# Performance work log

Hardware: AMD Instinct MI355X
Metric: run time of the kernel (lower is better)

The kernel has to match this reference:

```python
import jax, jax.numpy as jnp
import numpy as np

N = 100000   # nodes
E = 1000000  # edges
F_IN = 128
H = 64
L = 6
C = 10
G = 64       # graphs in batch


def setup_inputs() -> dict:
    key = jax.random.key(0)
    ks = jax.random.split(key, 12)
    x = jax.random.normal(ks[0], (N, F_IN), dtype=jnp.float32)
    edge_index = jax.random.randint(ks[1], (2, E), 0, N, dtype=jnp.int64)
    batch = jnp.sort(jax.random.randint(ks[2], (N,), 0, G, dtype=jnp.int64))
    s = lambda fan: 1.0 / np.sqrt(fan)
    return {
        "x": x,
        "edge_index": edge_index,
        "batch": batch,
        "W0": jax.random.normal(ks[3], (F_IN, H), dtype=jnp.float32) * s(F_IN),
        "b0": jnp.zeros((H,), jnp.float32),
        "Wh": jax.random.normal(ks[4], (L - 1, H, H), dtype=jnp.float32) * s(H),
        "bh": jnp.zeros((L - 1, H), jnp.float32),
        "jkW": jax.random.normal(ks[5], (H * L, H), dtype=jnp.float32) * s(H * L),
        "jkb": jnp.zeros((H,), jnp.float32),
        "W1": jax.random.normal(ks[6], (H, H), dtype=jnp.float32) * s(H),
        "b1": jnp.zeros((H,), jnp.float32),
        "W2": jax.random.normal(ks[7], (H, C), dtype=jnp.float32) * s(H),
        "b2": jnp.zeros((C,), jnp.float32),
    }


def reference(x, edge_index, batch, W0, b0, Wh, bh, jkW, jkb, W1, b1, W2, b2):
    n = x.shape[0]
    # add self-loops (PyG GCNConv default)
    loops = jnp.arange(n, dtype=edge_index.dtype)
    src = jnp.concatenate([edge_index[0], loops])
    dst = jnp.concatenate([edge_index[1], loops])
    # symmetric degree normalization D^{-1/2} (A+I) D^{-1/2}
    deg = jax.ops.segment_sum(jnp.ones_like(dst, x.dtype), dst, num_segments=n)
    disq = jnp.where(deg > 0, deg ** -0.5, 0.0)
    norm = (disq[src] * disq[dst])[:, None]  # [E+N, 1]

    def gcn(h, W, b):
        hW = h @ W                              # [N, H] transform first
        msg = hW[src] * norm                    # gather + normalize
        agg = jax.ops.segment_sum(msg, dst, num_segments=n)  # scatter-add
        return agg + b

    h = jax.nn.relu(gcn(x, W0, b0))
    xs = [h]
    for i in range(L - 1):
        h = jax.nn.relu(gcn(h, Wh[i], bh[i]))
        xs.append(h)
    hcat = jnp.concatenate(xs, axis=-1)         # JK 'cat' -> [N, H*L]
    h = jax.nn.relu(hcat @ jkW + jkb)
    pooled = jax.ops.segment_sum(h, batch, num_segments=G)  # global_add_pool
    h = jax.nn.relu(pooled @ W1 + b1)
    return jax.nn.softmax(h @ W2 + b2, axis=-1)  # [G, C]
```

## Files before the change

### kernel.cpp

```cpp
#include <hip/hip_runtime.h>
#include <hip/hip_fp16.h>

#define NN 100000
#define NE 1000000
#define F_INF 128
#define HID 64
#define NLAY 6
#define NCLS 10
#define NGRAPH 64
#define PART_SZ 12500
#define SCAT_BLKS (((NE + 2047) / 2048) * 8)
#define GEMM_GRID ((NN + 63) / 64)

typedef float floatx2 __attribute__((ext_vector_type(2)));

__device__ __forceinline__ float4 h4f(ushort4 u) {
    __half2 lo = *reinterpret_cast<__half2*>(&u);
    __half2 hi = *reinterpret_cast<__half2*>(reinterpret_cast<unsigned short*>(&u) + 2);
    float2 a = __half22float2(lo);
    float2 b = __half22float2(hi);
    return make_float4(a.x, a.y, b.x, b.y);
}

__device__ __forceinline__ ushort4 f4h(float4 v) {
    __half2 lo = __floats2half2_rn(v.x, v.y);
    __half2 hi = __floats2half2_rn(v.z, v.w);
    ushort4 u;
    *reinterpret_cast<__half2*>(&u) = lo;
    *reinterpret_cast<__half2*>(reinterpret_cast<unsigned short*>(&u) + 2) = hi;
    return u;
}

__device__ __forceinline__ unsigned f4_fp8(float4 v) {
    unsigned w = 0;
    w = __builtin_amdgcn_cvt_pk_fp8_f32(v.x, v.y, w, false);
    w = __builtin_amdgcn_cvt_pk_fp8_f32(v.z, v.w, w, true);
    return w;
}

__device__ __forceinline__ void accf8(unsigned u, float4& a) {
    floatx2 lo = __builtin_amdgcn_cvt_pk_f32_fp8(u, false);
    floatx2 hi = __builtin_amdgcn_cvt_pk_f32_fp8(u, true);
    a.x += lo[0]; a.y += lo[1]; a.z += hi[0]; a.w += hi[1];
}

__global__ void k_hist(const int* __restrict__ dst, int* __restrict__ counts, int e) {
    int i0 = blockIdx.x * 1024 + threadIdx.x;
    #pragma unroll
    for (int k = 0; k < 4; k++) {
        int i = i0 + k * 256;
        if (i < e) atomicAdd(&counts[dst[i]], 1);
    }
}

__global__ void k_blocksum(const int* __restrict__ counts, int* __restrict__ bsum, int n) {
    int i = blockIdx.x * 256 + threadIdx.x;
    int v = (i < n) ? counts[i] : 0;
    #pragma unroll
    for (int off = 32; off >= 1; off >>= 1) v += __shfl_down(v, off);
    __shared__ int ws[4];
    if ((threadIdx.x & 63) == 0) ws[threadIdx.x >> 6] = v;
    __syncthreads();
    if (threadIdx.x == 0) bsum[blockIdx.x] = ws[0] + ws[1] + ws[2] + ws[3];
}

__global__ void k_scanbsum(int* __restrict__ bsum, int nb) {
    __shared__ int sh[512];
    int t = threadIdx.x;
    int v = (t < nb) ? bsum[t] : 0;
    sh[t] = v; __syncthreads();
    for (int off = 1; off < 512; off <<= 1) {
        int x = (t >= off) ? sh[t - off] : 0;
        __syncthreads();
        sh[t] += x; __syncthreads();
    }
    if (t < nb) bsum[t] = sh[t] - v;
}

__global__ void k_scanwrite(const int* __restrict__ counts, const int* __restrict__ bsumx,
                            int* __restrict__ rowptr, int* __restrict__ wptr,
                            float* __restrict__ disq, int n, int e) {
    __shared__ int sh[256];
    int t = threadIdx.x;
    int i = blockIdx.x * 256 + t;
    int v = (i < n) ? counts[i] : 0;
    sh[t] = v; __syncthreads();
    for (int off = 1; off < 256; off <<= 1) {
        int x = (t >= off) ? sh[t - off] : 0;
        __syncthreads();
        sh[t] += x; __syncthreads();
    }
    int excl = sh[t] - v + bsumx[blockIdx.x];
    if (i < n) {
        rowptr[i] = excl;
        wptr[i]   = excl;
        disq[i]   = rsqrtf((float)(v + 1));
    }
    if (i == 0) rowptr[n] = e;
}

__global__ __launch_bounds__(256) void k_scatter_gemm0(
    const int* __restrict__ src, const int* __restrict__ dst,
    int* __restrict__ wptr, int* __restrict__ csr, int e,
    const float* __restrict__ x, const float* __restrict__ W0,
    const float* __restrict__ disq, unsigned* __restrict__ C8, int n)
{
    __shared__ float Ws[32 * 64];
    __shared__ float As[64 * 36];

    if (blockIdx.x >= GEMM_GRID) {
        int sbid = blockIdx.x - GEMM_GRID;
        int part = sbid & 7;
        int i0 = (sbid >> 3) * 2048 + threadIdx.x;
        #pragma unroll
        for (int k = 0; k < 8; k++) {
            int i = i0 + k * 256;
            if (i < e) {
                int d = dst[i];
                if (d / PART_SZ == part) {
                    int pos = atomicAdd(&wptr[d], 1);
                    csr[pos] = src[i];
                }
            }
        }
        return;
    }

    const int tid  = threadIdx.x;
    const int col4 = (tid & 15) * 4;
    const int rowq = tid >> 4;
    const int base = blockIdx.x * 64;
    const int ar   = tid >> 3;
    const int ac4  = (tid & 7) * 4;

    float4 wreg[2], areg[2];
    #pragma unroll
    for (int i = 0; i < 2; i++)
        wreg[i] = *(const float4*)(W0 + (size_t)(i * 256 + tid) * 4);
    #pragma unroll
    for (int rr = 0; rr < 2; rr++) {
        int row = base + ar + rr * 32;
        areg[rr] = make_float4(0.f, 0.f, 0.f, 0.f);
        if (row < n) areg[rr] = *(const float4*)(x + (size_t)row * F_INF + ac4);
    }
    #pragma unroll
    for (int i = 0; i < 2; i++)
        *(float4*)(Ws + (size_t)(i * 256 + tid) * 4) = wreg[i];
    #pragma unroll
    for (int rr = 0; rr < 2; rr++)
        *(float4*)(As + (size_t)(ar + rr * 32) * 36 + ac4) = areg[rr];
    __syncthreads();

    float4 acc[4];
    #pragma unroll
    for (int r = 0; r < 4; r++) acc[r] = make_float4(0.f, 0.f, 0.f, 0.f);

    for (int k0 = 0; k0 < F_INF; k0 += 32) {
        const bool more = (k0 + 32) < F_INF;
        if (more) {
            #pragma unroll
            for (int i = 0; i < 2; i++)
                wreg[i] = *(const float4*)(W0 + (size_t)(k0 + 32) * 64 + (i * 256 + tid) * 4);
            #pragma unroll
            for (int rr = 0; rr < 2; rr++) {
                int row = base + ar + rr * 32;
                areg[rr] = make_float4(0.f, 0.f, 0.f, 0.f);
                if (row < n) areg[rr] = *(const float4*)(x + (size_t)row * F_INF + k0 + 32 + ac4);
            }
        }
        #pragma unroll 8
        for (int k = 0; k < 32; k++) {
            float4 w = *(const float4*)(Ws + k * 64 + col4);
            float a0 = As[(rowq * 4 + 0) * 36 + k];
            float a1 = As[(rowq * 4 + 1) * 36 + k];
            float a2 = As[(rowq * 4 + 2) * 36 + k];
            float a3 = As[(rowq * 4 + 3) * 36 + k];
            acc[0].x = fmaf(a0, w.x, acc[0].x); acc[0].y = fmaf(a0, w.y, acc[0].y);
            acc[0].z = fmaf(a0, w.z, acc[0].z); acc[0].w = fmaf(a0, w.w, acc[0].w);
            acc[1].x = fmaf(a1, w.x, acc[1].x); acc[1].y = fmaf(a1, w.y, acc[1].y);
            acc[1].z = fmaf(a1, w.z, acc[1].z); acc[1].w = fmaf(a1, w.w, acc[1].w);
            acc[2].x = fmaf(a2, w.x, acc[2].x); acc[2].y = fmaf(a2, w.y, acc[2].y);
            acc[2].z = fmaf(a2, w.z, acc[2].z); acc[2].w = fmaf(a2, w.w, acc[2].w);
            acc[3].x = fmaf(a3, w.x, acc[3].x); acc[3].y = fmaf(a3, w.y, acc[3].y);
            acc[3].z = fmaf(a3, w.z, acc[3].z); acc[3].w = fmaf(a3, w.w, acc[3].w);
        }
        __syncthreads();
        if (more) {
            #pragma unroll
            for (int i = 0; i < 2; i++)
                *(float4*)(Ws + (size_t)(i * 256 + tid) * 4) = wreg[i];
            #pragma unroll
            for (int rr = 0; rr < 2; rr++)
                *(float4*)(As + (size_t)(ar + rr * 32) * 36 + ac4) = areg[rr];
            __syncthreads();
        }
    }

    #pragma unroll
    for (int r = 0; r < 4; r++) {
        int row = base + rowq * 4 + r;
        if (row < n) {
            float s = disq[row];
            float4 o;
            o.x = acc[r].x * s; o.y = acc[r].y * s;
            o.z = acc[r].z * s; o.w = acc[r].w * s;
            C8[(size_t)row * 16 + (tid & 15)] = f4_fp8(o);
        }
    }
}

__global__ __launch_bounds__(256) void k_gemm_dual(
    const unsigned short* __restrict__ A16,
    const float* __restrict__ W,
    const float* __restrict__ jkw,
    const float* __restrict__ disq,
    unsigned* __restrict__ C8,
    unsigned short* __restrict__ jkacc16,
    int jk_mode, int n)
{
    __shared__ float Ws[64 * 64];
    __shared__ float Ws2[64 * 64];
    __shared__ float As[64 * 68];
    const int tid  = threadIdx.x;
    const int col4 = (tid & 15) * 4;
    const int rowq = tid >> 4;
    const int base = blockIdx.x * 64;

    #pragma unroll
    for (int i = 0; i < 4; i++) {
        float4 v = *(const float4*)(W + (size_t)(i * 256 + tid) * 4);
        *(float4*)(Ws + (size_t)(i * 256 + tid) * 4) = v;
        float4 v2 = *(const float4*)(jkw + (size_t)(i * 256 + tid) * 4);
        *(float4*)(Ws2 + (size_t)(i * 256 + tid) * 4) = v2;
    }
    {
        const ushort4* Ah = (const ushort4*)A16;
        #pragma unroll
        for (int rr = 0; rr < 4; rr++) {
            int row = base + rowq + rr * 16;
            float4 v = make_float4(0.f, 0.f, 0.f, 0.f);
            if (row < n) v = h4f(Ah[(size_t)row * 16 + (tid & 15)]);
            *(float4*)(As + (size_t)(rowq + rr * 16) * 68 + col4) = v;
        }
    }
    __syncthreads();

    float4 acc[4], acc2[4];
    #pragma unroll
    for (int r = 0; r < 4; r++) {
        acc[r]  = make_float4(0.f, 0.f, 0.f, 0.f);
        acc2[r] = make_float4(0.f, 0.f, 0.f, 0.f);
    }

    #pragma unroll 4
    for (int k = 0; k < 64; k++) {
        float4 w  = *(const float4*)(Ws  + k * 64 + col4);
        float4 w2 = *(const float4*)(Ws2 + k * 64 + col4);
        float a0 = As[(rowq * 4 + 0) * 68 + k];
        float a1 = As[(rowq * 4 + 1) * 68 + k];
        float a2 = As[(rowq * 4 + 2) * 68 + k];
        float a3 = As[(rowq * 4 + 3) * 68 + k];
        acc[0].x = fmaf(a0, w.x, acc[0].x); acc[0].y = fmaf(a0, w.y, acc[0].y);
        acc[0].z = fmaf(a0, w.z, acc[0].z); acc[0].w = fmaf(a0, w.w, acc[0].w);
        acc[1].x = fmaf(a1, w.x, acc[1].x); acc[1].y = fmaf(a1, w.y, acc[1].y);
        acc[1].z = fmaf(a1, w.z, acc[1].z); acc[1].w = fmaf(a1, w.w, acc[1].w);
        acc[2].x = fmaf(a2, w.x, acc[2].x); acc[2].y = fmaf(a2, w.y, acc[2].y);
        acc[2].z = fmaf(a2, w.z, acc[2].z); acc[2].w = fmaf(a2, w.w, acc[2].w);
        acc[3].x = fmaf(a3, w.x, acc[3].x); acc[3].y = fmaf(a3, w.y, acc[3].y);
        acc[3].z = fmaf(a3, w.z, acc[3].z); acc[3].w = fmaf(a3, w.w, acc[3].w);
        acc2[0].x = fmaf(a0, w2.x, acc2[0].x); acc2[0].y = fmaf(a0, w2.y, acc2[0].y);
        acc2[0].z = fmaf(a0, w2.z, acc2[0].z); acc2[0].w = fmaf(a0, w2.w, acc2[0].w);
        acc2[1].x = fmaf(a1, w2.x, acc2[1].x); acc2[1].y = fmaf(a1, w2.y, acc2[1].y);
        acc2[1].z = fmaf(a1, w2.z, acc2[1].z); acc2[1].w = fmaf(a1, w2.w, acc2[1].w);
        acc2[2].x = fmaf(a2, w2.x, acc2[2].x); acc2[2].y = fmaf(a2, w2.y, acc2[2].y);
        acc2[2].z = fmaf(a2, w2.z, acc2[2].z); acc2[2].w = fmaf(a2, w2.w, acc2[2].w);
        acc2[3].x = fmaf(a3, w2.x, acc2[3].x); acc2[3].y = fmaf(a3, w2.y, acc2[3].y);
        acc2[3].z = fmaf(a3, w2.z, acc2[3].z); acc2[3].w = fmaf(a3, w2.w, acc2[3].w);
    }

    #pragma unroll
    for (int r = 0; r < 4; r++) {
        int row = base + rowq * 4 + r;
        if (row < n) {
            float s = disq[row];
            float4 o;
            o.x = acc[r].x * s; o.y = acc[r].y * s;
            o.z = acc[r].z * s; o.w = acc[r].w * s;
            C8[(size_t)row * 16 + (tid & 15)] = f4_fp8(o);
            if (jk_mode == 1) {
                ((ushort4*)jkacc16)[(size_t)row * 16 + (tid & 15)] = f4h(acc2[r]);
            } else {
                float4 p = h4f(((const ushort4*)jkacc16)[(size_t)row * 16 + (tid & 15)]);
                p.x += acc2[r].x; p.y += acc2[r].y;
                p.z += acc2[r].z; p.w += acc2[r].w;
                ((ushort4*)jkacc16)[(size_t)row * 16 + (tid & 15)] = f4h(p);
            }
        }
    }
}

__global__ __launch_bounds__(256) void k_gather(
    const int* __restrict__ rowptr, const int* __restrict__ csr,
    const unsigned* __restrict__ hW8, const float* __restrict__ disq,
    const float* __restrict__ bias, unsigned short* __restrict__ hout16, int n)
{
    int wid  = (blockIdx.x * 256 + threadIdx.x) >> 6;
    if (wid >= n) return;
    int lane = threadIdx.x & 63;
    int fb = lane & 15;
    int es = lane >> 4;
    int j  = rowptr[wid];
    int r1 = rowptr[wid + 1];
    float4 v  = make_float4(0.f, 0.f, 0.f, 0.f);
    float4 v2 = make_float4(0.f, 0.f, 0.f, 0.f);
    if (es == 0) accf8(hW8[(size_t)wid * 16 + fb], v);
    while (j < r1) {
        int cnt = min(r1 - j, 64);
        int idx = (lane < cnt) ? csr[j + lane] : 0;
        for (int jj = 0; jj < cnt; jj += 16) {
            int i0 = jj + es, i1 = jj + 4 + es, i2 = jj + 8 + es, i3 = jj + 12 + es;
            int s0 = __shfl(idx, i0 & 63);
            int s1 = __shfl(idx, i1 & 63);
            int s2 = __shfl(idx, i2 & 63);
            int s3 = __shfl(idx, i3 & 63);
            unsigned t0 = hW8[(size_t)s0 * 16 + fb];
            unsigned t1 = hW8[(size_t)s1 * 16 + fb];
            unsigned t2 = hW8[(size_t)s2 * 16 + fb];
            unsigned t3 = hW8[(size_t)s3 * 16 + fb];
            if (i0 < cnt) accf8(t0, v);
            if (i1 < cnt) accf8(t1, v2);
            if (i2 < cnt) accf8(t2, v);
            if (i3 < cnt) accf8(t3, v2);
        }
        j += cnt;
    }
    v.x += v2.x; v.y += v2.y; v.z += v2.z; v.w += v2.w;
    v.x += __shfl_xor(v.x, 16); v.y += __shfl_xor(v.y, 16);
    v.z += __shfl_xor(v.z, 16); v.w += __shfl_xor(v.w, 16);
    v.x += __shfl_xor(v.x, 32); v.y += __shfl_xor(v.y, 32);
    v.z += __shfl_xor(v.z, 32); v.w += __shfl_xor(v.w, 32);
    if (es == 0) {
        float s = disq[wid];
        float4 b = ((const float4*)bias)[fb];
        float4 o;
        o.x = fmaxf(fmaf(s, v.x, b.x), 0.f);
        o.y = fmaxf(fmaf(s, v.y, b.y), 0.f);
        o.z = fmaxf(fmaf(s, v.z, b.z), 0.f);
        o.w = fmaxf(fmaf(s, v.w, b.w), 0.f);
        ((ushort4*)hout16)[(size_t)wid * 16 + fb] = f4h(o);
    }
}

__global__ __launch_bounds__(256) void k_jkfin_pool(
    const unsigned short* __restrict__ A16,
    const float* __restrict__ W,
    const unsigned short* __restrict__ jkacc16,
    const float* __restrict__ bias,
    const int* __restrict__ batch,
    float* __restrict__ pooled,
    int n)
{
    __shared__ float Ws[64 * 64];
    __shared__ float As[64 * 68];
    const int tid  = threadIdx.x;
    const int col4 = (tid & 15) * 4;
    const int rowq = tid >> 4;
    const int base = blockIdx.x * 64;

    #pragma unroll
    for (int i = 0; i < 4; i++) {
        float4 v = *(const float4*)(W + (size_t)(i * 256 + tid) * 4);
        *(float4*)(Ws + (size_t)(i * 256 + tid) * 4) = v;
    }
    {
        const ushort4* Ah = (const ushort4*)A16;
        #pragma unroll
        for (int rr = 0; rr < 4; rr++) {
            int row = base + rowq + rr * 16;
            float4 v = make_float4(0.f, 0.f, 0.f, 0.f);
            if (row < n) v = h4f(Ah[(size_t)row * 16 + (tid & 15)]);
            *(float4*)(As + (size_t)(rowq + rr * 16) * 68 + col4) = v;
        }
    }
    __syncthreads();

    float4 acc[4];
    #pragma unroll
    for (int r = 0; r < 4; r++) acc[r] = make_float4(0.f, 0.f, 0.f, 0.f);
    #pragma unroll 8
    for (int k = 0; k < 64; k++) {
        float4 w = *(const float4*)(Ws + k * 64 + col4);
        float a0 = As[(rowq * 4 + 0) * 68 + k];
        float a1 = As[(rowq * 4 + 1) * 68 + k];
        float a2 = As[(rowq * 4 + 2) * 68 + k];
        float a3 = As[(rowq * 4 + 3) * 68 + k];
        acc[0].x = fmaf(a0, w.x, acc[0].x); acc[0].y = fmaf(a0, w.y, acc[0].y);
        acc[0].z = fmaf(a0, w.z, acc[0].z); acc[0].w = fmaf(a0, w.w, acc[0].w);
        acc[1].x = fmaf(a1, w.x, acc[1].x); acc[1].y = fmaf(a1, w.y, acc[1].y);
        acc[1].z = fmaf(a1, w.z, acc[1].z); acc[1].w = fmaf(a1, w.w, acc[1].w);
        acc[2].x = fmaf(a2, w.x, acc[2].x); acc[2].y = fmaf(a2, w.y, acc[2].y);
        acc[2].z = fmaf(a2, w.z, acc[2].z); acc[2].w = fmaf(a2, w.w, acc[2].w);
        acc[3].x = fmaf(a3, w.x, acc[3].x); acc[3].y = fmaf(a3, w.y, acc[3].y);
        acc[3].z = fmaf(a3, w.z, acc[3].z); acc[3].w = fmaf(a3, w.w, acc[3].w);
    }
    __syncthreads();

    float* slab = Ws;
    #pragma unroll
    for (int i = tid; i < 4096; i += 256) slab[i] = 0.f;
    __syncthreads();

    float4 bb = *(const float4*)(bias + col4);
    int curg = -1;
    float4 s4 = make_float4(0.f, 0.f, 0.f, 0.f);
    #pragma unroll
    for (int r = 0; r < 4; r++) {
        int row = base + rowq * 4 + r;
        if (row < n) {
            float4 p = h4f(((const ushort4*)jkacc16)[(size_t)row * 16 + (tid & 15)]);
            float4 vv;
            vv.x = fmaxf(acc[r].x + p.x + bb.x, 0.f);
            vv.y = fmaxf(acc[r].y + p.y + bb.y, 0.f);
            vv.z = fmaxf(acc[r].z + p.z + bb.z, 0.f);
            vv.w = fmaxf(acc[r].w + p.w + bb.w, 0.f);
            int g = batch[row];
            if (g != curg) {
                if (curg >= 0) {
                    atomicAdd(&slab[curg * 64 + col4 + 0], s4.x);
                    atomicAdd(&slab[curg * 64 + col4 + 1], s4.y);
                    atomicAdd(&slab[curg * 64 + col4 + 2], s4.z);
                    atomicAdd(&slab[curg * 64 + col4 + 3], s4.w);
                }
                curg = g; s4 = vv;
            } else {
                s4.x += vv.x; s4.y += vv.y; s4.z += vv.z; s4.w += vv.w;
            }
        }
    }
    if (curg >= 0) {
        atomicAdd(&slab[curg * 64 + col4 + 0], s4.x);
        atomicAdd(&slab[curg * 64 + col4 + 1], s4.y);
        atomicAdd(&slab[curg * 64 + col4 + 2], s4.z);
        atomicAdd(&slab[curg * 64 + col4 + 3], s4.w);
    }
    __syncthreads();

    int g0 = batch[base];
    int g1 = batch[(base + 63 < n) ? (base + 63) : (n - 1)];
    int cnt = (g1 - g0 + 1) * 64;
    for (int i = tid; i < cnt; i += 256) {
        int g = g0 + (i >> 6);
        int c = i & 63;
        float v = slab[g * 64 + c];
        if (v != 0.f) atomicAdd(&pooled[g * 64 + c], v);
    }
}

__global__ __launch_bounds__(64) void k_head(
    const float* __restrict__ pooled,
    const float* __restrict__ W1, const float* __restrict__ b1,
    const float* __restrict__ W2, const float* __restrict__ b2,
    float* __restrict__ out)
{
    __shared__ float p[64];
    __shared__ float h1[64];
    __shared__ float lg[16];
    const int g = blockIdx.x;
    const int t = threadIdx.x;

    p[t] = pooled[g * 64 + t];
    __syncthreads();

    float acc = b1[t];
    #pragma unroll 8
    for (int k = 0; k < 64; k++) acc = fmaf(p[k], W1[k * 64 + t], acc);
    h1[t] = fmaxf(acc, 0.f);
    __syncthreads();

    if (t < NCLS) {
        float a = b2[t];
        #pragma unroll 8
        for (int j = 0; j < 64; j++) a = fmaf(h1[j], W2[j * NCLS + t], a);
        lg[t] = a;
    }
    __syncthreads();

    if (t == 0) {
        float mx = lg[0];
        #pragma unroll
        for (int c = 1; c < NCLS; c++) mx = fmaxf(mx, lg[c]);
        float ssum = 0.f;
        float e[NCLS];
        #pragma unroll
        for (int c = 0; c < NCLS; c++) { e[c] = __expf(lg[c] - mx); ssum += e[c]; }
        float inv = 1.0f / ssum;
        #pragma unroll
        for (int c = 0; c < NCLS; c++) out[g * NCLS + c] = e[c] * inv;
    }
}

extern "C" void kernel_launch(void* const* d_in, const int* in_sizes, int n_in,
                              void* d_out, int out_size, void* d_ws, size_t ws_size,
                              hipStream_t stream) {
    (void)in_sizes; (void)n_in; (void)out_size; (void)ws_size;
    const float* x     = (const float*)d_in[0];
    const int*   ei    = (const int*)d_in[1];
    const int*   batch = (const int*)d_in[2];
    const float* W0    = (const float*)d_in[3];
    const float* b0    = (const float*)d_in[4];
    const float* Wh    = (const float*)d_in[5];
    const float* bh    = (const float*)d_in[6];
    const float* jkW   = (const float*)d_in[7];
    const float* jkb   = (const float*)d_in[8];
    const float* W1    = (const float*)d_in[9];
    const float* b1    = (const float*)d_in[10];
    const float* W2    = (const float*)d_in[11];
    const float* b2    = (const float*)d_in[12];

    const int* src = ei;
    const int* dst = ei + NE;

    float*          fws     = (float*)d_ws;
    float*          disq    = fws;
    unsigned*       hWb8    = (unsigned*)(disq + 100352);
    unsigned short* h16     = (unsigned short*)(hWb8 + (size_t)NN * 16);
    unsigned short* jkacc16 = h16 + (size_t)NN * 64;
    float*          pooled  = (float*)(jkacc16 + (size_t)NN * 64);
    int*            counts  = (int*)(pooled + 4096);
    int*            rowptr  = counts + 100352;
    int*            wptr    = rowptr + 100352;
    int*            bsum    = wptr + 100352;
    int*            csr     = bsum + 512;

    const int NB_N = (NN + 255) / 256;

    hipMemsetAsync(counts, 0, (size_t)NN * sizeof(int), stream);
    k_hist<<<(NE + 1023) / 1024, 256, 0, stream>>>(dst, counts, NE);
    k_blocksum<<<NB_N, 256, 0, stream>>>(counts, bsum, NN);
    k_scanbsum<<<1, 512, 0, stream>>>(bsum, NB_N);
    k_scanwrite<<<NB_N, 256, 0, stream>>>(counts, bsum, rowptr, wptr, disq, NN, NE);

    k_scatter_gemm0<<<GEMM_GRID + SCAT_BLKS, 256, 0, stream>>>(
        src, dst, wptr, csr, NE, x, W0, disq, hWb8, NN);

    const int gather_grid = (NN + 3) / 4;
    k_gather<<<gather_grid, 256, 0, stream>>>(rowptr, csr, hWb8, disq, b0, h16, NN);
    for (int l = 1; l < NLAY; l++) {
        const float* W   = Wh + (size_t)(l - 1) * 64 * 64;
        const float* jw  = jkW + (size_t)(l - 1) * 64 * 64;
        int          jkm = (l == 1) ? 1 : 2;
        k_gemm_dual<<<GEMM_GRID, 256, 0, stream>>>(h16, W, jw, disq, hWb8, jkacc16, jkm, NN);
        k_gather<<<gather_grid, 256, 0, stream>>>(rowptr, csr, hWb8, disq,
                                                  bh + (size_t)(l - 1) * 64, h16, NN);
    }

    hipMemsetAsync(pooled, 0, 64 * 64 * sizeof(float), stream);
    k_jkfin_pool<<<GEMM_GRID, 256, 0, stream>>>(h16, jkW + (size_t)5 * 64 * 64, jkacc16,
                                                jkb, batch, pooled, NN);
    k_head<<<NGRAPH, 64, 0, stream>>>(pooled, W1, b1, W2, b2, (float*)d_out);
}
```

Baseline: 496.7 us.

## Use bf16 MFMA for per-layer dual GEMM with pre-transposed bf16 weights

```diff
diff --git a/kernel.cpp b/kernel.cpp
--- a/kernel.cpp
+++ b/kernel.cpp
@@ -13,6 +13,8 @@
 #define GEMM_GRID ((NN + 63) / 64)
 
 typedef float floatx2 __attribute__((ext_vector_type(2)));
+typedef short bf16x8 __attribute__((ext_vector_type(8)));
+typedef float f32x4 __attribute__((ext_vector_type(4)));
 
 __device__ __forceinline__ float4 h4f(ushort4 u) {
     __half2 lo = *reinterpret_cast<__half2*>(&u);
@@ -31,13 +33,29 @@
     return u;
 }
 
+__device__ __forceinline__ unsigned short f2bf(float f) {
+    unsigned u = __float_as_uint(f);
+    u += 0x7FFF + ((u >> 16) & 1);
+    return (unsigned short)(u >> 16);
+}
+__device__ __forceinline__ float bf2f(unsigned short h) {
+    return __uint_as_float(((unsigned)h) << 16);
+}
+__device__ __forceinline__ ushort4 f4bf(float4 v) {
+    ushort4 u;
+    u.x = f2bf(v.x); u.y = f2bf(v.y); u.z = f2bf(v.z); u.w = f2bf(v.w);
+    return u;
+}
+__device__ __forceinline__ float4 bf4f(ushort4 u) {
+    return make_float4(bf2f(u.x), bf2f(u.y), bf2f(u.z), bf2f(u.w));
+}
+
 __device__ __forceinline__ unsigned f4_fp8(float4 v) {
     unsigned w = 0;
     w = __builtin_amdgcn_cvt_pk_fp8_f32(v.x, v.y, w, false);
     w = __builtin_amdgcn_cvt_pk_fp8_f32(v.z, v.w, w, true);
     return w;
 }
-
 __device__ __forceinline__ void accf8(unsigned u, float4& a) {
     floatx2 lo = __builtin_amdgcn_cvt_pk_f32_fp8(u, false);
     floatx2 hi = __builtin_amdgcn_cvt_pk_f32_fp8(u, true);
@@ -97,6 +115,17 @@
         disq[i]   = rsqrtf((float)(v + 1));
     }
     if (i == 0) rowptr[n] = e;
+}
+
+__global__ void k_cvtw(const float* __restrict__ Wh, const float* __restrict__ jkW,
+                       unsigned short* __restrict__ WtAll) {
+    int i = blockIdx.x * 256 + threadIdx.x;
+    if (i >= 11 * 4096) return;
+    int m = i >> 12;
+    int r = (i >> 6) & 63;
+    int c = i & 63;
+    const float* srcm = (m < 5) ? (Wh + (size_t)m * 4096) : (jkW + (size_t)(m - 5) * 4096);
+    WtAll[i] = f2bf(srcm[c * 64 + r]);
 }
 
 __global__ __launch_bounds__(256) void k_scatter_gemm0(
@@ -209,90 +238,89 @@
     }
 }
 
-__global__ __launch_bounds__(256) void k_gemm_dual(
-    const unsigned short* __restrict__ A16,
-    const float* __restrict__ W,
-    const float* __restrict__ jkw,
+__global__ __launch_bounds__(256) void k_gemm_dual_mfma(
+    const unsigned short* __restrict__ Abf,
+    const unsigned short* __restrict__ Wt,
+    const unsigned short* __restrict__ jkWt,
     const float* __restrict__ disq,
     unsigned* __restrict__ C8,
     unsigned short* __restrict__ jkacc16,
     int jk_mode, int n)
 {
-    __shared__ float Ws[64 * 64];
-    __shared__ float Ws2[64 * 64];
-    __shared__ float As[64 * 68];
+    __shared__ float Cs[64 * 68];
     const int tid  = threadIdx.x;
+    const int lane = tid & 63;
+    const int wave = tid >> 6;
+    const int base = blockIdx.x * 64;
+    const int rtl  = lane & 15;
+    const int kg   = lane >> 4;
+
+    int arow = base + wave * 16 + rtl;
+    bf16x8 a0 = {0, 0, 0, 0, 0, 0, 0, 0}, a1 = a0;
+    if (arow < n) {
+        a0 = *(const bf16x8*)(Abf + (size_t)arow * 64 + kg * 8);
+        a1 = *(const bf16x8*)(Abf + (size_t)arow * 64 + 32 + kg * 8);
+    }
+
+    f32x4 acc[4], acc2[4];
+    #pragma unroll
+    for (int c = 0; c < 4; c++) {
+        bf16x8 b0 = *(const bf16x8*)(Wt   + (size_t)(c * 16 + rtl) * 64 + kg * 8);
+        bf16x8 b1 = *(const bf16x8*)(Wt   + (size_t)(c * 16 + rtl) * 64 + 32 + kg * 8);
+        bf16x8 j0 = *(const bf16x8*)(jkWt + (size_t)(c * 16 + rtl) * 64 + kg * 8);
+        bf16x8 j1 = *(const bf16x8*)(jkWt + (size_t)(c * 16 + rtl) * 64 + 32 + kg * 8);
+        f32x4 z = {0.f, 0.f, 0.f, 0.f};
+        acc[c]  = __builtin_amdgcn_mfma_f32_16x16x32_bf16(a0, b0, z, 0, 0, 0);
+        acc[c]  = __builtin_amdgcn_mfma_f32_16x16x32_bf16(a1, b1, acc[c], 0, 0, 0);
+        acc2[c] = __builtin_amdgcn_mfma_f32_16x16x32_bf16(a0, j0, z, 0, 0, 0);
+        acc2[c] = __builtin_amdgcn_mfma_f32_16x16x32_bf16(a1, j1, acc2[c], 0, 0, 0);
+    }
+
+    #pragma unroll
+    for (int c = 0; c < 4; c++)
+        #pragma unroll
+        for (int r = 0; r < 4; r++)
+            Cs[(wave * 16 + kg * 4 + r) * 68 + c * 16 + rtl] = acc[c][r];
+    __syncthreads();
+
+    const int rowq = tid >> 4;
     const int col4 = (tid & 15) * 4;
-    const int rowq = tid >> 4;
-    const int base = blockIdx.x * 64;
-
-    #pragma unroll
-    for (int i = 0; i < 4; i++) {
-        float4 v = *(const float4*)(W + (size_t)(i * 256 + tid) * 4);
-        *(float4*)(Ws + (size_t)(i * 256 + tid) * 4) = v;
-        float4 v2 = *(const float4*)(jkw + (size_t)(i * 256 + tid) * 4);
-        *(float4*)(Ws2 + (size_t)(i * 256 + tid) * 4) = v2;
-    }
-    {
-        const ushort4* Ah = (const ushort4*)A16;
-        #pragma unroll
-        for (int rr = 0; rr < 4; rr++) {
-            int row = base + rowq + rr * 16;
-            float4 v = make_float4(0.f, 0.f, 0.f, 0.f);
-            if (row < n) v = h4f(Ah[(size_t)row * 16 + (tid & 15)]);
-            *(float4*)(As + (size_t)(rowq + rr * 16) * 68 + col4) = v;
-        }
-    }
-    __syncthreads();
-
-    float4 acc[4], acc2[4];
-    #pragma unroll
-    for (int r = 0; r < 4; r++) {
-        acc[r]  = make_float4(0.f, 0.f, 0.f, 0.f);
-        acc2[r] = make_float4(0.f, 0.f, 0.f, 0.f);
-    }
-
-    #pragma unroll 4
-    for (int k = 0; k < 64; k++) {
-        float4 w  = *(const float4*)(Ws  + k * 64 + col4);
-        float4 w2 = *(const float4*)(Ws2 + k * 64 + col4);
-        float a0 = As[(rowq * 4 + 0) * 68 + k];
-        float a1 = As[(rowq * 4 + 1) * 68 + k];
-        float a2 = As[(rowq * 4 + 2) * 68 + k];
-        float a3 = As[(rowq * 4 + 3) * 68 + k];
-        acc[0].x = fmaf(a0, w.x, acc[0].x); acc[0].y = fmaf(a0, w.y, acc[0].y);
-        acc[0].z = fmaf(a0, w.z, acc[0].z); acc[0].w = fmaf(a0, w.w, acc[0].w);
-        acc[1].x = fmaf(a1, w.x, acc[1].x); acc[1].y = fmaf(a1, w.y, acc[1].y);
-        acc[1].z = fmaf(a1, w.z, acc[1].z); acc[1].w = fmaf(a1, w.w, acc[1].w);
-        acc[2].x = fmaf(a2, w.x, acc[2].x); acc[2].y = fmaf(a2, w.y, acc[2].y);
-        acc[2].z = fmaf(a2, w.z, acc[2].z); acc[2].w = fmaf(a2, w.w, acc[2].w);
-        acc[3].x = fmaf(a3, w.x, acc[3].x); acc[3].y = fmaf(a3, w.y, acc[3].y);
-        acc[3].z = fmaf(a3, w.z, acc[3].z); acc[3].w = fmaf(a3, w.w, acc[3].w);
-        acc2[0].x = fmaf(a0, w2.x, acc2[0].x); acc2[0].y = fmaf(a0, w2.y, acc2[0].y);
-        acc2[0].z = fmaf(a0, w2.z, acc2[0].z); acc2[0].w = fmaf(a0, w2.w, acc2[0].w);
-        acc2[1].x = fmaf(a1, w2.x, acc2[1].x); acc2[1].y = fmaf(a1, w2.y, acc2[1].y);
-        acc2[1].z = fmaf(a1, w2.z, acc2[1].z); acc2[1].w = fmaf(a1, w2.w, acc2[1].w);
-        acc2[2].x = fmaf(a2, w2.x, acc2[2].x); acc2[2].y = fmaf(a2, w2.y, acc2[2].y);
-        acc2[2].z = fmaf(a2, w2.z, acc2[2].z); acc2[2].w = fmaf(a2, w2.w, acc2[2].w);
-        acc2[3].x = fmaf(a3, w2.x, acc2[3].x); acc2[3].y = fmaf(a3, w2.y, acc2[3].y);
-        acc2[3].z = fmaf(a3, w2.z, acc2[3].z); acc2[3].w = fmaf(a3, w2.w, acc2[3].w);
-    }
-
     #pragma unroll
     for (int r = 0; r < 4; r++) {
         int row = base + rowq * 4 + r;
         if (row < n) {
             float s = disq[row];
             float4 o;
-            o.x = acc[r].x * s; o.y = acc[r].y * s;
-            o.z = acc[r].z * s; o.w = acc[r].w * s;
+            o.x = Cs[(rowq * 4 + r) * 68 + col4 + 0] * s;
+            o.y = Cs[(rowq * 4 + r) * 68 + col4 + 1] * s;
+            o.z = Cs[(rowq * 4 + r) * 68 + col4 + 2] * s;
+            o.w = Cs[(rowq * 4 + r) * 68 + col4 + 3] * s;
             C8[(size_t)row * 16 + (tid & 15)] = f4_fp8(o);
+        }
+    }
+    __syncthreads();
+
+    #pragma unroll
+    for (int c = 0; c < 4; c++)
+        #pragma unroll
+        for (int r = 0; r < 4; r++)
+            Cs[(wave * 16 + kg * 4 + r) * 68 + c * 16 + rtl] = acc2[c][r];
+    __syncthreads();
+
+    #pragma unroll
+    for (int r = 0; r < 4; r++) {
+        int row = base + rowq * 4 + r;
+        if (row < n) {
+            float4 q;
+            q.x = Cs[(rowq * 4 + r) * 68 + col4 + 0];
+            q.y = Cs[(rowq * 4 + r) * 68 + col4 + 1];
+            q.z = Cs[(rowq * 4 + r) * 68 + col4 + 2];
+            q.w = Cs[(rowq * 4 + r) * 68 + col4 + 3];
             if (jk_mode == 1) {
-                ((ushort4*)jkacc16)[(size_t)row * 16 + (tid & 15)] = f4h(acc2[r]);
+                ((ushort4*)jkacc16)[(size_t)row * 16 + (tid & 15)] = f4h(q);
             } else {
                 float4 p = h4f(((const ushort4*)jkacc16)[(size_t)row * 16 + (tid & 15)]);
-                p.x += acc2[r].x; p.y += acc2[r].y;
-                p.z += acc2[r].z; p.w += acc2[r].w;
+                p.x += q.x; p.y += q.y; p.z += q.z; p.w += q.w;
                 ((ushort4*)jkacc16)[(size_t)row * 16 + (tid & 15)] = f4h(p);
             }
         }
@@ -302,7 +330,7 @@
 __global__ __launch_bounds__(256) void k_gather(
     const int* __restrict__ rowptr, const int* __restrict__ csr,
     const unsigned* __restrict__ hW8, const float* __restrict__ disq,
-    const float* __restrict__ bias, unsigned short* __restrict__ hout16, int n)
+    const float* __restrict__ bias, unsigned short* __restrict__ houtbf, int n)
 {
     int wid  = (blockIdx.x * 256 + threadIdx.x) >> 6;
     if (wid >= n) return;
@@ -347,12 +375,12 @@
         o.y = fmaxf(fmaf(s, v.y, b.y), 0.f);
         o.z = fmaxf(fmaf(s, v.z, b.z), 0.f);
         o.w = fmaxf(fmaf(s, v.w, b.w), 0.f);
-        ((ushort4*)hout16)[(size_t)wid * 16 + fb] = f4h(o);
+        ((ushort4*)houtbf)[(size_t)wid * 16 + fb] = f4bf(o);
     }
 }
 
 __global__ __launch_bounds__(256) void k_jkfin_pool(
-    const unsigned short* __restrict__ A16,
+    const unsigned short* __restrict__ Abf,
     const float* __restrict__ W,
     const unsigned short* __restrict__ jkacc16,
     const float* __restrict__ bias,
@@ -373,12 +401,12 @@
         *(float4*)(Ws + (size_t)(i * 256 + tid) * 4) = v;
     }
     {
-        const ushort4* Ah = (const ushort4*)A16;
+        const ushort4* Ah = (const ushort4*)Abf;
         #pragma unroll
         for (int rr = 0; rr < 4; rr++) {
             int row = base + rowq + rr * 16;
             float4 v = make_float4(0.f, 0.f, 0.f, 0.f);
-            if (row < n) v = h4f(Ah[(size_t)row * 16 + (tid & 15)]);
+            if (row < n) v = bf4f(Ah[(size_t)row * 16 + (tid & 15)]);
             *(float4*)(As + (size_t)(rowq + rr * 16) * 68 + col4) = v;
         }
     }
@@ -523,16 +551,19 @@
     float*          fws     = (float*)d_ws;
     float*          disq    = fws;
     unsigned*       hWb8    = (unsigned*)(disq + 100352);
-    unsigned short* h16     = (unsigned short*)(hWb8 + (size_t)NN * 16);
-    unsigned short* jkacc16 = h16 + (size_t)NN * 64;
+    unsigned short* hbf     = (unsigned short*)(hWb8 + (size_t)NN * 16);
+    unsigned short* jkacc16 = hbf + (size_t)NN * 64;
     float*          pooled  = (float*)(jkacc16 + (size_t)NN * 64);
     int*            counts  = (int*)(pooled + 4096);
     int*            rowptr  = counts + 100352;
     int*            wptr    = rowptr + 100352;
     int*            bsum    = wptr + 100352;
     int*            csr     = bsum + 512;
+    unsigned short* wtbf    = (unsigned short*)(csr + NE);
 
     const int NB_N = (NN + 255) / 256;
+
+    k_cvtw<<<(11 * 4096 + 255) / 256, 256, 0, stream>>>(Wh, jkW, wtbf);
 
     hipMemsetAsync(counts, 0, (size_t)NN * sizeof(int), stream);
     k_hist<<<(NE + 1023) / 1024, 256, 0, stream>>>(dst, counts, NE);
@@ -544,18 +575,19 @@
         src, dst, wptr, csr, NE, x, W0, disq, hWb8, NN);
 
     const int gather_grid = (NN + 3) / 4;
-    k_gather<<<gather_grid, 256, 0, stream>>>(rowptr, csr, hWb8, disq, b0, h16, NN);
+    k_gather<<<gather_grid, 256, 0, stream>>>(rowptr, csr, hWb8, disq, b0, hbf, NN);
     for (int l = 1; l < NLAY; l++) {
-        const float* W   = Wh + (size_t)(l - 1) * 64 * 64;
-        const float* jw  = jkW + (size_t)(l - 1) * 64 * 64;
-        int          jkm = (l == 1) ? 1 : 2;
-        k_gemm_dual<<<GEMM_GRID, 256, 0, stream>>>(h16, W, jw, disq, hWb8, jkacc16, jkm, NN);
+        const unsigned short* Wt  = wtbf + (size_t)(l - 1) * 4096;
+        const unsigned short* jwt = wtbf + (size_t)(5 + l - 1) * 4096;
+        int jkm = (l == 1) ? 1 : 2;
+        k_gemm_dual_mfma<<<GEMM_GRID, 256, 0, stream>>>(hbf, Wt, jwt, disq,
+                                                        hWb8, jkacc16, jkm, NN);
         k_gather<<<gather_grid, 256, 0, stream>>>(rowptr, csr, hWb8, disq,
-                                                  bh + (size_t)(l - 1) * 64, h16, NN);
+                                                  bh + (size_t)(l - 1) * 64, hbf, NN);
     }
 
     hipMemsetAsync(pooled, 0, 64 * 64 * sizeof(float), stream);
-    k_jkfin_pool<<<GEMM_GRID, 256, 0, stream>>>(h16, jkW + (size_t)5 * 64 * 64, jkacc16,
+    k_jkfin_pool<<<GEMM_GRID, 256, 0, stream>>>(hbf, jkW + (size_t)5 * 64 * 64, jkacc16,
                                                 jkb, batch, pooled, NN);
     k_head<<<NGRAPH, 64, 0, stream>>>(pooled, W1, b1, W2, b2, (float*)d_out);
 }
```

Measured after the change: 460.3 us. 1.08x faster.
